# Kernel tuning notes

Hardware: AMD Instinct MI355X
Metric: run time of the kernel (lower is better)

The kernel has to match this reference:

```python
import jax, jax.numpy as jnp
import numpy as np

NS, NA = 50000, 50000
ES, EA = 1000000, 500000
XD, UD, HD, MH = 8, 8, 64, 64


def _mlp_params(key, d_in, d_h, d_out):
    ks = jax.random.split(key, 3)
    s = 0.05
    return (jax.random.normal(ks[0], (d_in, d_h), jnp.float32) * s, jnp.zeros((d_h,), jnp.float32),
            jax.random.normal(ks[1], (d_h, d_h), jnp.float32) * s, jnp.zeros((d_h,), jnp.float32),
            jax.random.normal(ks[2], (d_h, d_out), jnp.float32) * s, jnp.zeros((d_out,), jnp.float32))


def _mlp(z, w1, b1, w2, b2, w3, b3):
    z = jnp.tanh(z @ w1 + b1)
    z = jnp.tanh(z @ w2 + b2)
    return z @ w3 + b3


def setup_inputs() -> dict:
    key = jax.random.key(0)
    ks = jax.random.split(key, 12)
    inp = {
        'pos_state': jax.random.uniform(ks[0], (NS, 2), jnp.float32),
        'pos_action': jax.random.uniform(ks[1], (NA, 2), jnp.float32),
        'h': jax.random.normal(ks[2], (NS, HD), jnp.float32),
        'x': jax.random.normal(ks[3], (NS, XD), jnp.float32),
        'u': jax.random.normal(ks[4], (NA, UD), jnp.float32),
        'a2s_src': jax.random.randint(ks[5], (EA,), 0, NA, jnp.int32),
        'a2s_dst': jax.random.randint(ks[6], (EA,), 0, NS, jnp.int32),
        'a2s_dis': jax.random.uniform(ks[7], (EA, 1), jnp.float32),
        's2s_src': jax.random.randint(ks[8], (ES,), 0, NS, jnp.int32),
        's2s_dst': jax.random.randint(ks[9], (ES,), 0, NS, jnp.int32),
        's2s_dis': jax.random.uniform(ks[10], (ES, 1), jnp.float32),
    }
    pk = jax.random.split(ks[11], 3)
    u2h = _mlp_params(pk[0], 2 * 2 + 1 + UD, MH, HD)
    x2h = _mlp_params(pk[1], 2 * 2 + 1 + XD + HD, MH, HD)
    upd = _mlp_params(pk[2], 2 + 3 * HD + XD, MH, HD)
    for pref, p in (('u2h', u2h), ('x2h', x2h), ('upd', upd)):
        for i, (w, b) in enumerate(zip(p[0::2], p[1::2]), 1):
            inp[f'{pref}_w{i}'] = w
            inp[f'{pref}_b{i}'] = b
    return inp


def reference(pos_state, pos_action, h, x, u,
              a2s_src, a2s_dst, a2s_dis, s2s_src, s2s_dst, s2s_dis,
              u2h_w1, u2h_b1, u2h_w2, u2h_b2, u2h_w3, u2h_b3,
              x2h_w1, x2h_b1, x2h_w2, x2h_b2, x2h_w3, x2h_b3,
              upd_w1, upd_b1, upd_w2, upd_b2, upd_w3, upd_b3):
    ns = pos_state.shape[0]
    # a2s: gather action src / state dst, per-edge MLP, sum into dst state nodes
    msg_u_in = jnp.concatenate([pos_action[a2s_src], pos_state[a2s_dst], a2s_dis, u[a2s_src]], axis=-1)
    msg_u = _mlp(msg_u_in, u2h_w1, u2h_b1, u2h_w2, u2h_b2, u2h_w3, u2h_b3)  # [EA, HD]
    sum_u = jax.ops.segment_sum(msg_u, a2s_dst, num_segments=ns)
    # s2s: gather state src/dst, per-edge MLP, mean into dst state nodes
    msg_x_in = jnp.concatenate([pos_state[s2s_src], pos_state[s2s_dst], s2s_dis, x[s2s_src], h[s2s_src]], axis=-1)
    msg_x = _mlp(msg_x_in, x2h_w1, x2h_b1, x2h_w2, x2h_b2, x2h_w3, x2h_b3)  # [ES, HD]
    sum_x = jax.ops.segment_sum(msg_x, s2s_dst, num_segments=ns)
    deg = jax.ops.segment_sum(jnp.ones((s2s_dst.shape[0],), jnp.float32), s2s_dst, num_segments=ns)
    mean_x = sum_x / jnp.maximum(deg, 1.0)[:, None]  # DGL mean: 0 for zero in-degree
    # node update MLP
    upd_in = jnp.concatenate([pos_state, h, sum_u, mean_x, x], axis=-1)
    return _mlp(upd_in, upd_w1, upd_b1, upd_w2, upd_b2, upd_w3, upd_b3)
```

## Files before the change

### kernel.cpp

```cpp
#include <hip/hip_runtime.h>
#include <hip/hip_bf16.h>


typedef __attribute__((ext_vector_type(8))) short short8;
typedef __attribute__((ext_vector_type(4))) float f32x4;

#define MFMA(a, b, c) __builtin_amdgcn_mfma_f32_16x16x32_bf16(a, b, c, 0, 0, 0)

union FU { short8 v; unsigned int d[4]; unsigned short us[8]; };

__device__ __forceinline__ unsigned short f2bf(float f) {
    unsigned u = __float_as_uint(f);
    u += 0x7fffu + ((u >> 16) & 1u);
    return (unsigned short)(u >> 16);
}
__device__ __forceinline__ unsigned int pk2(float a, float b) {
    float2 t; t.x = a; t.y = b;
    union { __hip_bfloat162 h; unsigned int u; } c;
    c.h = __float22bfloat162_rn(t);
    return c.u;
}
__device__ __forceinline__ float tanh_fast(float xv) {
    float t = __builtin_amdgcn_exp2f(xv * 2.8853900817779268f);
    return 1.0f - 2.0f * __builtin_amdgcn_rcpf(t + 1.0f);
}

template <typename KM>
__device__ void build_gfrags(const float* __restrict__ w, unsigned short* dst,
                             int nchunks, int gtid, int gstr, KM km) {
    int total = nchunks * 4 * 64;
    for (int f = gtid; f < total; f += gstr) {
        int lv = f & 63, nt = (f >> 6) & 3, c = f >> 8;
        int n = nt * 16 + (lv & 15);
        int kb = c * 32 + ((lv >> 4) << 3);
        unsigned short* o = dst + f * 8;
        #pragma unroll
        for (int j = 0; j < 8; ++j) {
            int sk = km(kb + j);
            o[j] = (sk >= 0) ? f2bf(w[sk * 64 + n]) : (unsigned short)0;
        }
    }
}

#define PERM_KM [](int k) -> int { return (k >> 2) + 16 * (k & 3); }

#define ZTRANS(Zw, accv)                                                       \
    _Pragma("unroll")                                                          \
    for (int r = 0; r < 4; ++r) {                                              \
        uint2 pv;                                                              \
        pv.x = pk2(tanh_fast(accv[0][r]), tanh_fast(accv[1][r]));              \
        pv.y = pk2(tanh_fast(accv[2][r]), tanh_fast(accv[3][r]));              \
        *(uint2*)((Zw) + ((q << 2) + r) * 72 + (m16 << 2)) = pv;               \
    }

__global__ __launch_bounds__(256) void prep1(
    const float* __restrict__ ps, const float* __restrict__ pa,
    const float* __restrict__ h, const float* __restrict__ x,
    const float* __restrict__ u,
    const int* __restrict__ s2s_dst, const int* __restrict__ a2s_dst,
    unsigned short* __restrict__ s_row, unsigned short* __restrict__ a_row,
    int* __restrict__ cnt_s, int* __restrict__ rank_s,
    int* __restrict__ cnt_a, int* __restrict__ rank_a,
    const float* __restrict__ s_w1, const float* __restrict__ s_w2, const float* __restrict__ s_w3,
    const float* __restrict__ a_w1, const float* __restrict__ a_w2, const float* __restrict__ a_w3,
    const float* __restrict__ u_w1, const float* __restrict__ u_w2, const float* __restrict__ u_w3,
    unsigned short* __restrict__ ts, unsigned short* __restrict__ ta,
    unsigned short* __restrict__ tu,
    int NS, int NA, int ES, int EA, int MAINB)
{
    int bid = blockIdx.x;
    if (bid >= MAINB) {
        int gtid = (bid - MAINB) * 256 + threadIdx.x;
        int gstr = (gridDim.x - MAINB) * 256;
        build_gfrags(s_w1, ts, 3, gtid, gstr, [](int k) -> int {
            if (k < 2)   return k;
            if (k < 74)  return k + 3;
            if (k < 80)  return -2;
            if (k < 82)  return k - 78;
            if (k == 82) return 4;
            return -2; });
        build_gfrags(s_w2, ts + 3 * 2048, 2, gtid, gstr, PERM_KM);
        build_gfrags(s_w3, ts + 5 * 2048, 2, gtid, gstr, PERM_KM);
        build_gfrags(a_w1, ta, 1, gtid, gstr, [](int k) -> int {
            if (k < 2)   return k;
            if (k < 10)  return k + 3;
            if (k < 16)  return -2;
            if (k < 18)  return k - 14;
            if (k == 18) return 4;
            return -2; });
        build_gfrags(a_w2, ta + 1 * 2048, 2, gtid, gstr, PERM_KM);
        build_gfrags(a_w3, ta + 3 * 2048, 2, gtid, gstr, PERM_KM);
        build_gfrags(u_w1, tu, 7, gtid, gstr, [](int k) -> int {
            if (k < 192) return k + 2;
            if (k < 194) return k - 192;
            if (k < 202) return k;
            return -2; });
        build_gfrags(u_w2, tu + 7 * 2048, 2, gtid, gstr, PERM_KM);
        build_gfrags(u_w3, tu + 9 * 2048, 2, gtid, gstr, PERM_KM);
        return;
    }

    int R0 = NS * 80, R1 = R0 + NA * 16, R2 = R1 + ES, R3 = R2 + EA;
    for (int i = bid * 256 + threadIdx.x; i < R3; i += MAINB * 256) {
        if (i < R0) {
            int n = i / 80, k = i - n * 80;
            float v = (k < 2) ? ps[n * 2 + k] : (k < 10) ? x[n * 8 + k - 2]
                    : (k < 74) ? h[n * 64 + k - 10] : 0.f;
            s_row[i] = f2bf(v);
        } else if (i < R1) {
            int j = i - R0; int a = j / 16, k = j - a * 16;
            float v = (k < 2) ? pa[a * 2 + k] : (k < 10) ? u[a * 8 + k - 2] : 0.f;
            a_row[j] = f2bf(v);
        } else if (i < R2) {
            int e = i - R1;
            rank_s[e] = atomicAdd(&cnt_s[s2s_dst[e]], 1);
        } else {
            int e = i - R2;
            rank_a[e] = atomicAdd(&cnt_a[a2s_dst[e]], 1);
        }
    }
}

#define SCAN_CHUNK 1024

__global__ __launch_bounds__(256) void scan_a(const int* __restrict__ cnt,
                                              int* __restrict__ bsum, int N2)
{
    __shared__ int red[256];
    int t = threadIdx.x;
    int base = blockIdx.x * SCAN_CHUNK + t * 4;
    int s = 0;
    #pragma unroll
    for (int j = 0; j < 4; ++j) { int i = base + j; if (i < N2) s += cnt[i]; }
    red[t] = s; __syncthreads();
    for (int d = 128; d > 0; d >>= 1) {
        if (t < d) red[t] += red[t + d];
        __syncthreads();
    }
    if (t == 0) bsum[blockIdx.x] = red[0];
}

__global__ __launch_bounds__(128) void scan_b(int* __restrict__ bsum, int NB)
{
    __shared__ int part[128];
    int t = threadIdx.x;
    int v = (t < NB) ? bsum[t] : 0;
    part[t] = v; __syncthreads();
    for (int d = 1; d < 128; d <<= 1) {
        int w = (t >= d) ? part[t - d] : 0;
        __syncthreads();
        part[t] += w;
        __syncthreads();
    }
    if (t < NB) bsum[t] = part[t] - v;
}

__global__ __launch_bounds__(256) void scan_c(const int* __restrict__ cnt,
                                              const int* __restrict__ bsum,
                                              int* __restrict__ off,
                                              int N2, int NS, int ES)
{
    __shared__ int part[256];
    int t = threadIdx.x;
    int base = blockIdx.x * SCAN_CHUNK + t * 4;
    int c[4]; int s = 0;
    #pragma unroll
    for (int j = 0; j < 4; ++j) { int i = base + j; c[j] = (i < N2) ? cnt[i] : 0; s += c[j]; }
    part[t] = s; __syncthreads();
    for (int d = 1; d < 256; d <<= 1) {
        int w = (t >= d) ? part[t - d] : 0;
        __syncthreads();
        part[t] += w;
        __syncthreads();
    }
    int run = bsum[blockIdx.x] + part[t] - s;
    #pragma unroll
    for (int j = 0; j < 4; ++j) {
        int i = base + j;
        if (i < N2) off[i] = run - ((i >= NS) ? ES : 0);
        run += c[j];
    }
}

__global__ __launch_bounds__(256) void scatter_sort2(
    const int* __restrict__ srcS, const int* __restrict__ dstS,
    const int* __restrict__ rankS, const int* __restrict__ offS,
    const float* __restrict__ disS,
    const int* __restrict__ srcA, const int* __restrict__ dstA,
    const int* __restrict__ rankA, const int* __restrict__ offA,
    const float* __restrict__ disA,
    int* __restrict__ ssrcS, int* __restrict__ sdstS, float* __restrict__ sdisS,
    int* __restrict__ ssrcA, int* __restrict__ sdstA, float* __restrict__ sdisA,
    int ES, int EA)
{
    int tot = ES + EA;
    for (int i = blockIdx.x * 256 + threadIdx.x; i < tot; i += gridDim.x * 256) {
        if (i < ES) {
            int d = dstS[i];
            int pos = offS[d] + rankS[i];
            ssrcS[pos] = srcS[i];
            sdstS[pos] = d;
            sdisS[pos] = disS[i];
        } else {
            int e = i - ES;
            int d = dstA[e];
            int pos = offA[d] + rankA[e];
            ssrcA[pos] = srcA[e];
            sdstA[pos] = d;
            sdisA[pos] = disA[e];
        }
    }
}

template <int C1, int RS>
__device__ __forceinline__ void edge_path(
    const unsigned short* __restrict__ row_tab,
    const int* __restrict__ ssrc, const int* __restrict__ sdst,
    const float* __restrict__ sdis, const float* __restrict__ ps,
    const unsigned short* WT,
    const float* __restrict__ b1, const float* __restrict__ b2,
    const float* __restrict__ b3,
    float* __restrict__ sums, int E, int bid0, int nb, int tid,
    unsigned short* Zbase)
{
    const unsigned short* W1 = WT;
    const unsigned short* W2 = WT + C1 * 2048;
    const unsigned short* W3 = WT + (C1 + 2) * 2048;

    int wid = tid >> 6, lane = tid & 63, m16 = lane & 15, q = lane >> 4;
    unsigned short* Zw = Zbase + wid * (16 * 72);

    float bb1[4], bb2[4], bb3[4];
    #pragma unroll
    for (int nt = 0; nt < 4; ++nt) {
        bb1[nt] = b1[nt * 16 + m16];
        bb2[nt] = b2[nt * 16 + m16];
        bb3[nt] = b3[nt * 16 + m16];
    }

    int T = E >> 5;
    for (int t = bid0 * 4 + wid; t < T; t += nb * 4) {
        int p0 = t * 32;
        int sp0 = p0 + ((m16 >> 2) << 3) + (m16 & 3);
        int sp1 = sp0 + 4;
        int s0 = ssrc[sp0], s1 = ssrc[sp1];
        int pb = p0 + (q << 3);
        int4 dq0 = *(const int4*)(sdst + pb);
        int4 dq1 = *(const int4*)(sdst + pb + 4);
        int dseq[8] = {dq0.x, dq0.y, dq0.z, dq0.w, dq1.x, dq1.y, dq1.z, dq1.w};

        uint2 ep[2];
        ep[0].x = 0; ep[0].y = 0; ep[1].x = 0; ep[1].y = 0;
        if (q == 2) {
            int dA = sdst[sp0], dB = sdst[sp1];
            float2 pA = *(const float2*)(ps + 2 * dA);
            float2 pB = *(const float2*)(ps + 2 * dB);
            float zA = sdis[sp0], zB = sdis[sp1];
            ep[0].x = pk2(pA.x, pA.y); ep[0].y = (unsigned)f2bf(zA) | (0x3F80u << 16);
            ep[1].x = pk2(pB.x, pB.y); ep[1].y = (unsigned)f2bf(zB) | (0x3F80u << 16);
        }

        FU Lb[2][C1];
        const unsigned short* rA = row_tab + (size_t)s0 * RS;
        const unsigned short* rB = row_tab + (size_t)s1 * RS;
        #pragma unroll
        for (int c = 0; c < C1; ++c) {
            int off = c * 32 + q * 8;
            bool valid = (c < C1 - 1) || (q < 2);
            if (valid) {
                Lb[0][c].v = *(const short8*)(rA + off);
                Lb[1][c].v = *(const short8*)(rB + off);
            } else {
                Lb[0][c].d[0] = ep[0].x; Lb[0][c].d[1] = ep[0].y; Lb[0][c].d[2] = 0; Lb[0][c].d[3] = 0;
                Lb[1][c].d[0] = ep[1].x; Lb[1][c].d[1] = ep[1].y; Lb[1][c].d[2] = 0; Lb[1][c].d[3] = 0;
            }
        }

        f32x4 acc1[2][4];
        #pragma unroll
        for (int mt = 0; mt < 2; ++mt)
            #pragma unroll
            for (int nt = 0; nt < 4; ++nt)
                acc1[mt][nt] = (f32x4){bb1[nt], bb1[nt], bb1[nt], bb1[nt]};
        #pragma unroll
        for (int c = 0; c < C1; ++c)
            #pragma unroll
            for (int nt = 0; nt < 4; ++nt) {
                short8 wf = *(const short8*)(W1 + ((c * 4 + nt) * 64 + lane) * 8);
                acc1[0][nt] = MFMA(Lb[0][c].v, wf, acc1[0][nt]);
                acc1[1][nt] = MFMA(Lb[1][c].v, wf, acc1[1][nt]);
            }

        f32x4 a3[2][4];
        #pragma unroll
        for (int mt = 0; mt < 2; ++mt) {
            ZTRANS(Zw, acc1[mt])
            FU A2[2];
            A2[0].v = *(const short8*)(Zw + m16 * 72 + 0 * 32 + q * 8);
            A2[1].v = *(const short8*)(Zw + m16 * 72 + 1 * 32 + q * 8);

            f32x4 a2[4];
            #pragma unroll
            for (int nt = 0; nt < 4; ++nt) {
                a2[nt] = (f32x4){bb2[nt], bb2[nt], bb2[nt], bb2[nt]};
                short8 w0 = *(const short8*)(W2 + ((0 * 4 + nt) * 64 + lane) * 8);
                short8 w1f = *(const short8*)(W2 + ((1 * 4 + nt) * 64 + lane) * 8);
                a2[nt] = MFMA(A2[0].v, w0, a2[nt]);
                a2[nt] = MFMA(A2[1].v, w1f, a2[nt]);
            }

            ZTRANS(Zw, a2)
            FU A3[2];
            A3[0].v = *(const short8*)(Zw + m16 * 72 + 0 * 32 + q * 8);
            A3[1].v = *(const short8*)(Zw + m16 * 72 + 1 * 32 + q * 8);

            #pragma unroll
            for (int nt = 0; nt < 4; ++nt) {
                a3[mt][nt] = (f32x4){bb3[nt], bb3[nt], bb3[nt], bb3[nt]};
                short8 w0 = *(const short8*)(W3 + ((0 * 4 + nt) * 64 + lane) * 8);
                short8 w1f = *(const short8*)(W3 + ((1 * 4 + nt) * 64 + lane) * 8);
                a3[mt][nt] = MFMA(A3[0].v, w0, a3[mt][nt]);
                a3[mt][nt] = MFMA(A3[1].v, w1f, a3[mt][nt]);
            }
        }

        #pragma unroll
        for (int j = 0; j < 8; ++j) {
            int mt = j >> 2, r = j & 3;
            bool merge = (j < 7) && (dseq[j] == dseq[j + 1]);
            if (merge) {
                int mt2 = (j + 1) >> 2, r2 = (j + 1) & 3;
                #pragma unroll
                for (int nt = 0; nt < 4; ++nt) a3[mt2][nt][r2] += a3[mt][nt][r];
            } else {
                float* pbase = sums + (size_t)dseq[j] * 64 + m16;
                #pragma unroll
                for (int nt = 0; nt < 4; ++nt)
                    unsafeAtomicAdd(pbase + nt * 16, a3[mt][nt][r]);
            }
        }
    }
}

__global__ __launch_bounds__(256) void edges_mfma(
    const unsigned short* __restrict__ s_row, const unsigned short* __restrict__ a_row,
    const int* __restrict__ ssS, const int* __restrict__ sdS, const float* __restrict__ szS,
    const int* __restrict__ ssA, const int* __restrict__ sdA, const float* __restrict__ szA,
    const unsigned short* __restrict__ wtS, const unsigned short* __restrict__ wtA,
    const float* __restrict__ sb1, const float* __restrict__ sb2, const float* __restrict__ sb3,
    const float* __restrict__ ab1, const float* __restrict__ ab2, const float* __restrict__ ab3,
    const float* __restrict__ ps,
    float* __restrict__ sum_x, float* __restrict__ sum_u,
    int ES, int EA, int SPLIT)
{
    __shared__ __align__(16) unsigned short WT[7 * 2048];
    __shared__ __align__(16) unsigned short Z[4][16 * 72];

    int tid = threadIdx.x, bid = blockIdx.x;
    bool is_s = bid < SPLIT;
    const unsigned short* wt = is_s ? wtS : wtA;
    int wtn = is_s ? 7 * 2048 : 5 * 2048;
    for (int i = tid * 8; i < wtn; i += 256 * 8)
        *(short8*)(WT + i) = *(const short8*)(wt + i);
    __syncthreads();

    if (is_s)
        edge_path<3, 80>(s_row, ssS, sdS, szS, ps, WT, sb1, sb2, sb3,
                         sum_x, ES, bid, SPLIT, tid, &Z[0][0]);
    else
        edge_path<1, 16>(a_row, ssA, sdA, szA, ps, WT, ab1, ab2, ab3,
                         sum_u, EA, bid - SPLIT, gridDim.x - SPLIT, tid, &Z[0][0]);
}

__global__ __launch_bounds__(256) void upd_mfma(
    const float* __restrict__ ps, const float* __restrict__ h,
    const float* __restrict__ x,
    const float* __restrict__ su, const float* __restrict__ sx,
    const int* __restrict__ cnt_s,
    const unsigned short* __restrict__ wtab,
    const float* __restrict__ b1, const float* __restrict__ b2,
    const float* __restrict__ b3,
    float* __restrict__ out, int NS)
{
    __shared__ __align__(16) unsigned short WT[11 * 2048];
    __shared__ __align__(16) unsigned short Z[4][16 * 72];

    int tid = threadIdx.x;
    for (int i = tid * 8; i < 11 * 2048; i += 256 * 8)
        *(short8*)(WT + i) = *(const short8*)(wtab + i);
    __syncthreads();

    const unsigned short* W1 = WT;
    const unsigned short* W2 = WT + 7 * 2048;
    const unsigned short* W3 = WT + 9 * 2048;

    int wid = tid >> 6, lane = tid & 63, m16 = lane & 15, q = lane >> 4;
    unsigned short* Zw = &Z[wid][0];

    float bb1[4], bb2[4], bb3[4];
    #pragma unroll
    for (int nt = 0; nt < 4; ++nt) {
        bb1[nt] = b1[nt * 16 + m16];
        bb2[nt] = b2[nt * 16 + m16];
        bb3[nt] = b3[nt * 16 + m16];
    }

    int T = NS >> 4;
    for (int t = blockIdx.x * 4 + wid; t < T; t += gridDim.x * 4) {
        int n0 = t * 16;
        int n = n0 + m16;
        float rd = __builtin_amdgcn_rcpf(fmaxf((float)cnt_s[n], 1.0f));

        FU A[7];
        const float* hp = h + (size_t)n * 64;
        const float* sup = su + (size_t)n * 64;
        const float* sxp = sx + (size_t)n * 64;
        #pragma unroll
        for (int c = 0; c < 6; ++c) {
            const float* src = (c < 2) ? hp : (c < 4) ? sup : sxp;
            int base = (c & 1) * 32 + q * 8;
            float4 f0 = *(const float4*)(src + base);
            float4 f1 = *(const float4*)(src + base + 4);
            if (c >= 4) {
                f0.x *= rd; f0.y *= rd; f0.z *= rd; f0.w *= rd;
                f1.x *= rd; f1.y *= rd; f1.z *= rd; f1.w *= rd;
            }
            A[c].d[0] = pk2(f0.x, f0.y); A[c].d[1] = pk2(f0.z, f0.w);
            A[c].d[2] = pk2(f1.x, f1.y); A[c].d[3] = pk2(f1.z, f1.w);
        }
        A[6].d[0] = 0; A[6].d[1] = 0; A[6].d[2] = 0; A[6].d[3] = 0;
        if (q == 0) {
            float2 pp = *(const float2*)(ps + 2 * n);
            float4 x0 = *(const float4*)(x + 8 * n);
            float2 x1 = *(const float2*)(x + 8 * n + 4);
            A[6].d[0] = pk2(pp.x, pp.y);
            A[6].d[1] = pk2(x0.x, x0.y);
            A[6].d[2] = pk2(x0.z, x0.w);
            A[6].d[3] = pk2(x1.x, x1.y);
        } else if (q == 1) {
            float2 x2 = *(const float2*)(x + 8 * n + 6);
            A[6].d[0] = pk2(x2.x, x2.y);
        }

        f32x4 acc1[4];
        #pragma unroll
        for (int nt = 0; nt < 4; ++nt)
            acc1[nt] = (f32x4){bb1[nt], bb1[nt], bb1[nt], bb1[nt]};
        #pragma unroll
        for (int c = 0; c < 7; ++c)
            #pragma unroll
            for (int nt = 0; nt < 4; ++nt) {
                short8 wf = *(const short8*)(W1 + ((c * 4 + nt) * 64 + lane) * 8);
                acc1[nt] = MFMA(A[c].v, wf, acc1[nt]);
            }

        ZTRANS(Zw, acc1)
        FU A2[2];
        A2[0].v = *(const short8*)(Zw + m16 * 72 + 0 * 32 + q * 8);
        A2[1].v = *(const short8*)(Zw + m16 * 72 + 1 * 32 + q * 8);

        f32x4 a2[4];
        #pragma unroll
        for (int nt = 0; nt < 4; ++nt) {
            a2[nt] = (f32x4){bb2[nt], bb2[nt], bb2[nt], bb2[nt]};
            short8 w0 = *(const short8*)(W2 + ((0 * 4 + nt) * 64 + lane) * 8);
            short8 w1f = *(const short8*)(W2 + ((1 * 4 + nt) * 64 + lane) * 8);
            a2[nt] = MFMA(A2[0].v, w0, a2[nt]);
            a2[nt] = MFMA(A2[1].v, w1f, a2[nt]);
        }

        ZTRANS(Zw, a2)
        FU A3[2];
        A3[0].v = *(const short8*)(Zw + m16 * 72 + 0 * 32 + q * 8);
        A3[1].v = *(const short8*)(Zw + m16 * 72 + 1 * 32 + q * 8);

        f32x4 a3[4];
        #pragma unroll
        for (int nt = 0; nt < 4; ++nt) {
            a3[nt] = (f32x4){bb3[nt], bb3[nt], bb3[nt], bb3[nt]};
            short8 w0 = *(const short8*)(W3 + ((0 * 4 + nt) * 64 + lane) * 8);
            short8 w1f = *(const short8*)(W3 + ((1 * 4 + nt) * 64 + lane) * 8);
            a3[nt] = MFMA(A3[0].v, w0, a3[nt]);
            a3[nt] = MFMA(A3[1].v, w1f, a3[nt]);
        }

        #pragma unroll
        for (int nt = 0; nt < 4; ++nt)
            #pragma unroll
            for (int r = 0; r < 4; ++r)
                out[(size_t)(n0 + (q << 2) + r) * 64 + nt * 16 + m16] = a3[nt][r];
    }
}

extern "C" void kernel_launch(void* const* d_in, const int* in_sizes, int n_in,
                              void* d_out, int out_size, void* d_ws, size_t ws_size,
                              hipStream_t stream) {
    const float* pos_state  = (const float*)d_in[0];
    const float* pos_action = (const float*)d_in[1];
    const float* h          = (const float*)d_in[2];
    const float* x          = (const float*)d_in[3];
    const float* u          = (const float*)d_in[4];
    const int*   a2s_src    = (const int*)d_in[5];
    const int*   a2s_dst    = (const int*)d_in[6];
    const float* a2s_dis    = (const float*)d_in[7];
    const int*   s2s_src    = (const int*)d_in[8];
    const int*   s2s_dst    = (const int*)d_in[9];
    const float* s2s_dis    = (const float*)d_in[10];
    const float* u2h_w1 = (const float*)d_in[11]; const float* u2h_b1 = (const float*)d_in[12];
    const float* u2h_w2 = (const float*)d_in[13]; const float* u2h_b2 = (const float*)d_in[14];
    const float* u2h_w3 = (const float*)d_in[15]; const float* u2h_b3 = (const float*)d_in[16];
    const float* x2h_w1 = (const float*)d_in[17]; const float* x2h_b1 = (const float*)d_in[18];
    const float* x2h_w2 = (const float*)d_in[19]; const float* x2h_b2 = (const float*)d_in[20];
    const float* x2h_w3 = (const float*)d_in[21]; const float* x2h_b3 = (const float*)d_in[22];
    const float* upd_w1 = (const float*)d_in[23]; const float* upd_b1 = (const float*)d_in[24];
    const float* upd_w2 = (const float*)d_in[25]; const float* upd_b2 = (const float*)d_in[26];
    const float* upd_w3 = (const float*)d_in[27]; const float* upd_b3 = (const float*)d_in[28];

    int NS = in_sizes[0] / 2;
    int NA = in_sizes[1] / 2;
    int EA = in_sizes[5];
    int ES = in_sizes[8];
    int N2 = 2 * NS;
    int NB = (N2 + SCAN_CHUNK - 1) / SCAN_CHUNK;

    char* p = (char*)d_ws;
    int*   cnt2  = (int*)p;            p += (size_t)N2 * 4;
    float* sum_u = (float*)p;          p += (size_t)NS * 64 * 4;
    float* sum_x = (float*)p;          p += (size_t)NS * 64 * 4;
    size_t zbytes = (size_t)(p - (char*)d_ws);
    int*   off2   = (int*)p;           p += (size_t)N2 * 4;
    int*   rank_s = (int*)p;           p += (size_t)ES * 4;
    int*   rank_a = (int*)p;           p += (size_t)EA * 4;
    int*   ssrc_s = (int*)p;           p += (size_t)ES * 4;
    int*   sdst_s = (int*)p;           p += (size_t)ES * 4;
    float* sdis_s = (float*)p;         p += (size_t)ES * 4;
    int*   ssrc_a = (int*)p;           p += (size_t)EA * 4;
    int*   sdst_a = (int*)p;           p += (size_t)EA * 4;
    float* sdis_a = (float*)p;         p += (size_t)EA * 4;
    unsigned short* s_row  = (unsigned short*)p; p += (size_t)NS * 80 * 2;
    unsigned short* a_row  = (unsigned short*)p; p += (size_t)NA * 16 * 2;
    int*   bsum   = (int*)p;           p += 128 * 4;
    unsigned short* wtab_s = (unsigned short*)p; p += 7 * 2048 * 2;
    unsigned short* wtab_a = (unsigned short*)p; p += 5 * 2048 * 2;
    unsigned short* wtab_u = (unsigned short*)p; p += 11 * 2048 * 2;
    (void)ws_size;

    int* cnt_s = cnt2;
    int* cnt_a = cnt2 + NS;
    int* off_s = off2;
    int* off_a = off2 + NS;

    hipMemsetAsync(d_ws, 0, zbytes, stream);

    const int MAINB = 2048;
    prep1<<<MAINB + 24, 256, 0, stream>>>(pos_state, pos_action, h, x, u,
                                          s2s_dst, a2s_dst, s_row, a_row,
                                          cnt_s, rank_s, cnt_a, rank_a,
                                          x2h_w1, x2h_w2, x2h_w3,
                                          u2h_w1, u2h_w2, u2h_w3,
                                          upd_w1, upd_w2, upd_w3,
                                          wtab_s, wtab_a, wtab_u,
                                          NS, NA, ES, EA, MAINB);
    scan_a<<<NB, 256, 0, stream>>>(cnt2, bsum, N2);
    scan_b<<<1, 128, 0, stream>>>(bsum, NB);
    scan_c<<<NB, 256, 0, stream>>>(cnt2, bsum, off2, N2, NS, ES);
    scatter_sort2<<<1024, 256, 0, stream>>>(s2s_src, s2s_dst, rank_s, off_s, s2s_dis,
                                            a2s_src, a2s_dst, rank_a, off_a, a2s_dis,
                                            ssrc_s, sdst_s, sdis_s,
                                            ssrc_a, sdst_a, sdis_a, ES, EA);
    edges_mfma<<<1536, 256, 0, stream>>>(s_row, a_row,
                                         ssrc_s, sdst_s, sdis_s,
                                         ssrc_a, sdst_a, sdis_a,
                                         wtab_s, wtab_a,
                                         x2h_b1, x2h_b2, x2h_b3,
                                         u2h_b1, u2h_b2, u2h_b3,
                                         pos_state, sum_x, sum_u,
                                         ES, EA, 1024);
    upd_mfma<<<784, 256, 0, stream>>>(pos_state, h, x, sum_u, sum_x, cnt_s,
                                      wtab_u, upd_b1, upd_b2, upd_b3,
                                      (float*)d_out, NS);
}
```

Baseline: 445.9 us.

## Pack edge src/dis as uint2, vectorize row packing, fuse sum zeroing into scatter

The sorted src index and distance are now stored together as one uint2 per edge, so the edge kernel reads them with a single load instead of two scattered ones. The bf16 row tables are built four elements per thread with 8-byte packed stores instead of one 2-byte store per element. Zeroing of the sum_u/sum_x accumulators moves from the host memset into the scatter kernel, so the memset only clears the counters. The s2s/a2s block split in the edge kernel is retuned from 1024 to 1120. In exchange, the scatter kernel does more work and its writes are wider.

```diff
diff --git a/kernel.cpp b/kernel.cpp
--- a/kernel.cpp
+++ b/kernel.cpp
@@ -100,17 +100,33 @@
         return;
     }
 
-    int R0 = NS * 80, R1 = R0 + NA * 16, R2 = R1 + ES, R3 = R2 + EA;
+    int R0 = NS * 32, R1 = R0 + NA * 4, R2 = R1 + ES, R3 = R2 + EA;
     for (int i = bid * 256 + threadIdx.x; i < R3; i += MAINB * 256) {
         if (i < R0) {
-            int n = i / 80, k = i - n * 80;
-            float v = (k < 2) ? ps[n * 2 + k] : (k < 10) ? x[n * 8 + k - 2]
-                    : (k < 74) ? h[n * 64 + k - 10] : 0.f;
-            s_row[i] = f2bf(v);
+            int n = i >> 5, kq = i & 31;
+            if (kq < 20) {
+                int k0 = kq << 2;
+                float f[4];
+                #pragma unroll
+                for (int j = 0; j < 4; ++j) {
+                    int k = k0 + j;
+                    f[j] = (k < 2) ? ps[n * 2 + k] : (k < 10) ? x[n * 8 + k - 2]
+                         : (k < 74) ? h[n * 64 + k - 10] : 0.f;
+                }
+                uint2 o; o.x = pk2(f[0], f[1]); o.y = pk2(f[2], f[3]);
+                *(uint2*)&s_row[(size_t)n * 80 + k0] = o;
+            }
         } else if (i < R1) {
-            int j = i - R0; int a = j / 16, k = j - a * 16;
-            float v = (k < 2) ? pa[a * 2 + k] : (k < 10) ? u[a * 8 + k - 2] : 0.f;
-            a_row[j] = f2bf(v);
+            int j2 = i - R0; int a = j2 >> 2, kq = j2 & 3;
+            int k0 = kq << 2;
+            float f[4];
+            #pragma unroll
+            for (int j = 0; j < 4; ++j) {
+                int k = k0 + j;
+                f[j] = (k < 2) ? pa[a * 2 + k] : (k < 10) ? u[a * 8 + k - 2] : 0.f;
+            }
+            uint2 o; o.x = pk2(f[0], f[1]); o.y = pk2(f[2], f[3]);
+            *(uint2*)&a_row[(size_t)a * 16 + k0] = o;
         } else if (i < R2) {
             int e = i - R1;
             rank_s[e] = atomicAdd(&cnt_s[s2s_dst[e]], 1);
@@ -189,25 +205,29 @@
     const int* __restrict__ srcA, const int* __restrict__ dstA,
     const int* __restrict__ rankA, const int* __restrict__ offA,
     const float* __restrict__ disA,
-    int* __restrict__ ssrcS, int* __restrict__ sdstS, float* __restrict__ sdisS,
-    int* __restrict__ ssrcA, int* __restrict__ sdstA, float* __restrict__ sdisA,
-    int ES, int EA)
-{
+    uint2* __restrict__ sdS, int* __restrict__ sdstS,
+    uint2* __restrict__ sdA, int* __restrict__ sdstA,
+    float* __restrict__ sums, int ES, int EA, int NZ4)
+{
+    int gtid = blockIdx.x * 256 + threadIdx.x;
+    int gstr = gridDim.x * 256;
+    for (int i = gtid; i < NZ4; i += gstr)
+        ((f32x4*)sums)[i] = (f32x4){0.f, 0.f, 0.f, 0.f};
     int tot = ES + EA;
-    for (int i = blockIdx.x * 256 + threadIdx.x; i < tot; i += gridDim.x * 256) {
+    for (int i = gtid; i < tot; i += gstr) {
         if (i < ES) {
             int d = dstS[i];
             int pos = offS[d] + rankS[i];
-            ssrcS[pos] = srcS[i];
+            uint2 v; v.x = (unsigned)srcS[i]; v.y = __float_as_uint(disS[i]);
+            sdS[pos] = v;
             sdstS[pos] = d;
-            sdisS[pos] = disS[i];
         } else {
             int e = i - ES;
             int d = dstA[e];
             int pos = offA[d] + rankA[e];
-            ssrcA[pos] = srcA[e];
+            uint2 v; v.x = (unsigned)srcA[e]; v.y = __float_as_uint(disA[e]);
+            sdA[pos] = v;
             sdstA[pos] = d;
-            sdisA[pos] = disA[e];
         }
     }
 }
@@ -215,8 +235,8 @@
 template <int C1, int RS>
 __device__ __forceinline__ void edge_path(
     const unsigned short* __restrict__ row_tab,
-    const int* __restrict__ ssrc, const int* __restrict__ sdst,
-    const float* __restrict__ sdis, const float* __restrict__ ps,
+    const uint2* __restrict__ srcdis, const int* __restrict__ sdst,
+    const float* __restrict__ ps,
     const unsigned short* WT,
     const float* __restrict__ b1, const float* __restrict__ b2,
     const float* __restrict__ b3,
@@ -243,7 +263,8 @@
         int p0 = t * 32;
         int sp0 = p0 + ((m16 >> 2) << 3) + (m16 & 3);
         int sp1 = sp0 + 4;
-        int s0 = ssrc[sp0], s1 = ssrc[sp1];
+        uint2 sd0 = srcdis[sp0], sd1 = srcdis[sp1];
+        int s0 = (int)sd0.x, s1 = (int)sd1.x;
         int pb = p0 + (q << 3);
         int4 dq0 = *(const int4*)(sdst + pb);
         int4 dq1 = *(const int4*)(sdst + pb + 4);
@@ -255,9 +276,10 @@
             int dA = sdst[sp0], dB = sdst[sp1];
             float2 pA = *(const float2*)(ps + 2 * dA);
             float2 pB = *(const float2*)(ps + 2 * dB);
-            float zA = sdis[sp0], zB = sdis[sp1];
-            ep[0].x = pk2(pA.x, pA.y); ep[0].y = (unsigned)f2bf(zA) | (0x3F80u << 16);
-            ep[1].x = pk2(pB.x, pB.y); ep[1].y = (unsigned)f2bf(zB) | (0x3F80u << 16);
+            ep[0].x = pk2(pA.x, pA.y);
+            ep[0].y = (unsigned)f2bf(__uint_as_float(sd0.y)) | (0x3F80u << 16);
+            ep[1].x = pk2(pB.x, pB.y);
+            ep[1].y = (unsigned)f2bf(__uint_as_float(sd1.y)) | (0x3F80u << 16);
         }
 
         FU Lb[2][C1];
@@ -344,8 +366,8 @@
 
 __global__ __launch_bounds__(256) void edges_mfma(
     const unsigned short* __restrict__ s_row, const unsigned short* __restrict__ a_row,
-    const int* __restrict__ ssS, const int* __restrict__ sdS, const float* __restrict__ szS,
-    const int* __restrict__ ssA, const int* __restrict__ sdA, const float* __restrict__ szA,
+    const uint2* __restrict__ sdS, const int* __restrict__ sdstS,
+    const uint2* __restrict__ sdA, const int* __restrict__ sdstA,
     const unsigned short* __restrict__ wtS, const unsigned short* __restrict__ wtA,
     const float* __restrict__ sb1, const float* __restrict__ sb2, const float* __restrict__ sb3,
     const float* __restrict__ ab1, const float* __restrict__ ab2, const float* __restrict__ ab3,
@@ -365,10 +387,10 @@
     __syncthreads();
 
     if (is_s)
-        edge_path<3, 80>(s_row, ssS, sdS, szS, ps, WT, sb1, sb2, sb3,
+        edge_path<3, 80>(s_row, sdS, sdstS, ps, WT, sb1, sb2, sb3,
                          sum_x, ES, bid, SPLIT, tid, &Z[0][0]);
     else
-        edge_path<1, 16>(a_row, ssA, sdA, szA, ps, WT, ab1, ab2, ab3,
+        edge_path<1, 16>(a_row, sdA, sdstA, ps, WT, ab1, ab2, ab3,
                          sum_u, EA, bid - SPLIT, gridDim.x - SPLIT, tid, &Z[0][0]);
 }
 
@@ -525,18 +547,16 @@
 
     char* p = (char*)d_ws;
     int*   cnt2  = (int*)p;            p += (size_t)N2 * 4;
+    size_t zbytes = (size_t)(p - (char*)d_ws);
     float* sum_u = (float*)p;          p += (size_t)NS * 64 * 4;
     float* sum_x = (float*)p;          p += (size_t)NS * 64 * 4;
-    size_t zbytes = (size_t)(p - (char*)d_ws);
     int*   off2   = (int*)p;           p += (size_t)N2 * 4;
     int*   rank_s = (int*)p;           p += (size_t)ES * 4;
     int*   rank_a = (int*)p;           p += (size_t)EA * 4;
-    int*   ssrc_s = (int*)p;           p += (size_t)ES * 4;
+    uint2* sd_s   = (uint2*)p;         p += (size_t)ES * 8;
     int*   sdst_s = (int*)p;           p += (size_t)ES * 4;
-    float* sdis_s = (float*)p;         p += (size_t)ES * 4;
-    int*   ssrc_a = (int*)p;           p += (size_t)EA * 4;
+    uint2* sd_a   = (uint2*)p;         p += (size_t)EA * 8;
     int*   sdst_a = (int*)p;           p += (size_t)EA * 4;
-    float* sdis_a = (float*)p;         p += (size_t)EA * 4;
     unsigned short* s_row  = (unsigned short*)p; p += (size_t)NS * 80 * 2;
     unsigned short* a_row  = (unsigned short*)p; p += (size_t)NA * 16 * 2;
     int*   bsum   = (int*)p;           p += 128 * 4;
@@ -566,16 +586,15 @@
     scan_c<<<NB, 256, 0, stream>>>(cnt2, bsum, off2, N2, NS, ES);
     scatter_sort2<<<1024, 256, 0, stream>>>(s2s_src, s2s_dst, rank_s, off_s, s2s_dis,
                                             a2s_src, a2s_dst, rank_a, off_a, a2s_dis,
-                                            ssrc_s, sdst_s, sdis_s,
-                                            ssrc_a, sdst_a, sdis_a, ES, EA);
+                                            sd_s, sdst_s, sd_a, sdst_a,
+                                            sum_u, ES, EA, NS * 32);
     edges_mfma<<<1536, 256, 0, stream>>>(s_row, a_row,
-                                         ssrc_s, sdst_s, sdis_s,
-                                         ssrc_a, sdst_a, sdis_a,
+                                         sd_s, sdst_s, sd_a, sdst_a,
                                          wtab_s, wtab_a,
                                          x2h_b1, x2h_b2, x2h_b3,
                                          u2h_b1, u2h_b2, u2h_b3,
                                          pos_state, sum_x, sum_u,
-                                         ES, EA, 1024);
+                                         ES, EA, 1120);
     upd_mfma<<<784, 256, 0, stream>>>(pos_state, h, x, sum_u, sum_x, cnt_s,
                                       wtab_u, upd_b1, upd_b2, upd_b3,
                                       (float*)d_out, NS);
```

Result: faster. 423.3 us (-5.1%).
